# Optimization experiments

Hardware: AMD Instinct MI355X
Metric: run time of the kernel (lower is better)

The kernel has to match this reference:

```python
import jax, jax.numpy as jnp
import numpy as np

IN_F = 256
OUT_F = 256
HOP = 3
ALPHA = 0.2   # LeakyReLU negative slope
BETA = 0.5    # hop mixing coefficient
N = 50000
E = 1600000


def setup_inputs() -> dict:
    key = jax.random.key(0)
    k1, k2, k3, k4 = jax.random.split(key, 4)
    inp = jax.random.normal(k1, (N, IN_F), dtype=jnp.float32)
    k_edge_list = jax.random.randint(k2, (HOP, 2, E), 0, N, dtype=jnp.int32)
    # xavier_normal-ish scales
    W = jax.random.normal(k3, (IN_F * HOP, OUT_F), dtype=jnp.float32) * (1.414 * np.sqrt(2.0 / (IN_F * HOP + OUT_F)))
    a = jax.random.normal(k4, (1, 2 * OUT_F * HOP), dtype=jnp.float32) * (1.414 * np.sqrt(2.0 / (1 + 2 * OUT_F * HOP)))
    return {"input": inp, "k_edge_list": k_edge_list, "W": W, "a": a}


def reference(input, k_edge_list, W, a):
    n = input.shape[0]
    h_prime_return = jnp.zeros((n, OUT_F), dtype=input.dtype)
    for i in range(HOP - 1, -1, -1):
        # per-hop projection: h = input @ W[i*in : (i+1)*in]  -> [N, OUT_F]
        h = input @ W[i * IN_F:(i + 1) * IN_F, :]
        src = k_edge_list[i, 0]  # [E] row indices (scatter targets)
        dst = k_edge_list[i, 1]  # [E] col indices (gather sources)
        ai = a[0, 2 * i * OUT_F:(2 * i + 2) * OUT_F]
        # a_i . cat(h[src], h[dst]) == (h @ a_src)[src] + (h @ a_dst)[dst]
        s_src = h @ ai[:OUT_F]   # [N]
        s_dst = h @ ai[OUT_F:]   # [N]
        score = s_src[src] + s_dst[dst]                     # [E]
        edge_e = jnp.exp(-jax.nn.leaky_relu(score, ALPHA))  # [E]
        # sparse row-sum: spmm(A, ones)
        e_rowsum = jax.ops.segment_sum(edge_e, src, num_segments=n)          # [N]
        # weighted aggregate: spmm(A, h)
        h_prime = jax.ops.segment_sum(edge_e[:, None] * h[dst], src, num_segments=n)  # [N, OUT_F]
        h_prime = h_prime / e_rowsum[:, None]
        h_prime_return = (1.0 - BETA) * h_prime + BETA * h_prime_return
    return jax.nn.elu(h_prime_return)  # concat=True path
```

## Files before the change

kernel.cpp:

```cpp
#include <hip/hip_runtime.h>

#define N_NODES 50000
#define E_EDGES 1600000
#define HOPS    3
#define KDIM    256
#define NOUT    768
#define MPAD    50048
#define NPS     50176
#define NCB     196
#define NCB_ALL (NCB * HOPS)
#define HSTRIDE ((size_t)MPAD * 256)
#define PCAP    10240
#define RCAP    9216
#define SEB     4096

typedef unsigned short u16;
typedef __bf16 bf16x8 __attribute__((ext_vector_type(8)));
typedef float  f32x4  __attribute__((ext_vector_type(4)));

__device__ __forceinline__ u16 f2bf(float f) {
  unsigned u = __float_as_uint(f);
  u += 0x7fffu + ((u >> 16) & 1u);
  return (u16)(u >> 16);
}
__device__ __forceinline__ float bf2f(u16 h) {
  return __uint_as_float(((unsigned)h) << 16);
}

__device__ __forceinline__ void gl2lds16(const void* g, void* l) {
  __builtin_amdgcn_global_load_lds(
      (__attribute__((address_space(1))) void*)(g),
      (__attribute__((address_space(3))) void*)(l), 16, 0, 0);
}

__global__ __launch_bounds__(256) void conv_a(const float* __restrict__ in,
                                              u16* __restrict__ A) {
  int idx  = blockIdx.x * 256 + threadIdx.x;
  int base = idx * 4;
  int row  = base >> 8;
  ushort4 o;
  if (row < N_NODES) {
    float4 v = *(const float4*)(in + base);
    o.x = f2bf(v.x); o.y = f2bf(v.y); o.z = f2bf(v.z); o.w = f2bf(v.w);
  } else {
    o.x = 0; o.y = 0; o.z = 0; o.w = 0;
  }
  *(ushort4*)(A + base) = o;
}

__global__ __launch_bounds__(256) void conv_w(const float* __restrict__ W,
                                              u16* __restrict__ Bt) {
  __shared__ float tile[32][33];
  int h  = blockIdx.z;
  int c0 = blockIdx.x * 32;
  int k0 = blockIdx.y * 32;
  int x  = threadIdx.x & 31;
  int y0 = threadIdx.x >> 5;
#pragma unroll
  for (int i = 0; i < 4; ++i) {
    int k = k0 + y0 + i * 8;
    tile[y0 + i * 8][x] = W[(size_t)(h * 256 + k) * 256 + (c0 + x)];
  }
  __syncthreads();
#pragma unroll
  for (int i = 0; i < 4; ++i) {
    int c = c0 + y0 + i * 8;
    Bt[(size_t)(h * 256 + c) * 256 + (k0 + x)] = f2bf(tile[x][y0 + i * 8]);
  }
}

__global__ __launch_bounds__(256) void gemm_kernel(const u16* __restrict__ A,
                                                   const u16* __restrict__ B,
                                                   u16* __restrict__ H,
                                                   const float* __restrict__ a,
                                                   float* __restrict__ ssrc,
                                                   float* __restrict__ sdst) {
  __shared__ char lds[32768];
  int tid  = threadIdx.x;
  int lane = tid & 63;
  int w    = tid >> 6;
  int wm   = w >> 1, wn = w & 1;
  int r    = lane & 15, q = lane >> 4;
  int bm   = blockIdx.y * 128, bn = blockIdx.x * 128;

  const u16* Ag0 = A + (size_t)(bm + 2 * w * 16 + r) * KDIM + q * 8;
  const u16* Bg0 = B + (size_t)(bn + 2 * w * 16 + r) * KDIM + q * 8;

  f32x4 zero = {0.f, 0.f, 0.f, 0.f};
  f32x4 acc[4][4];
#pragma unroll
  for (int mt = 0; mt < 4; ++mt)
#pragma unroll
    for (int nt = 0; nt < 4; ++nt) acc[mt][nt] = zero;

#define STAGE(b, kt)                                                      \
  do {                                                                    \
    int ko = (kt) * 32;                                                   \
    char* As_ = lds + (b) * 16384;                                        \
    char* Bs_ = As_ + 8192;                                               \
    gl2lds16(Ag0 + ko,             As_ + (2 * w) * 1024);                 \
    gl2lds16(Ag0 + 16 * KDIM + ko, As_ + (2 * w + 1) * 1024);             \
    gl2lds16(Bg0 + ko,             Bs_ + (2 * w) * 1024);                 \
    gl2lds16(Bg0 + 16 * KDIM + ko, Bs_ + (2 * w + 1) * 1024);             \
  } while (0)

  STAGE(0, 0);
  __syncthreads();

  for (int kt = 0; kt < 8; ++kt) {
    int cur = kt & 1;
    if (kt < 7) STAGE(cur ^ 1, kt + 1);
    char* As = lds + cur * 16384;
    char* Bs = As + 8192;
    bf16x8 af[4], bfv[4];
#pragma unroll
    for (int mt = 0; mt < 4; ++mt)
      af[mt] = *(const bf16x8*)(As + (wm * 4 + mt) * 1024 + lane * 16);
#pragma unroll
    for (int nt = 0; nt < 4; ++nt)
      bfv[nt] = *(const bf16x8*)(Bs + (wn * 4 + nt) * 1024 + lane * 16);
#pragma unroll
    for (int mt = 0; mt < 4; ++mt)
#pragma unroll
      for (int nt = 0; nt < 4; ++nt)
        acc[mt][nt] = __builtin_amdgcn_mfma_f32_16x16x32_bf16(
            af[mt], bfv[nt], acc[mt][nt], 0, 0, 0);
    if (kt < 7) __syncthreads();
  }
#undef STAGE

  int hop = bn >> 8;
  int cbase = (bn & 255) + wn * 64 + r;
  float asv[4], adv[4];
#pragma unroll
  for (int nt = 0; nt < 4; ++nt) {
    asv[nt] = a[hop * 512 + cbase + nt * 16];
    adv[nt] = a[hop * 512 + 256 + cbase + nt * 16];
  }
#pragma unroll
  for (int mt = 0; mt < 4; ++mt)
#pragma unroll
    for (int rg = 0; rg < 4; ++rg) {
      float ps = 0.f, pd = 0.f;
#pragma unroll
      for (int nt = 0; nt < 4; ++nt) {
        float v = acc[mt][nt][rg];
        ps += v * asv[nt];
        pd += v * adv[nt];
      }
#pragma unroll
      for (int m = 1; m < 16; m <<= 1) {
        ps += __shfl_xor(ps, m);
        pd += __shfl_xor(pd, m);
      }
      if (r == 0) {
        int row = bm + wm * 64 + mt * 16 + q * 4 + rg;
        if (row < N_NODES) {
          atomicAdd(&ssrc[hop * NPS + row], ps);
          atomicAdd(&sdst[hop * NPS + row], pd);
        }
      }
    }

#pragma unroll
  for (int mt = 0; mt < 4; ++mt)
#pragma unroll
    for (int nt = 0; nt < 4; ++nt)
#pragma unroll
      for (int rg = 0; rg < 4; ++rg) {
        int row = bm + wm * 64 + mt * 16 + q * 4 + rg;
        int col = bn + wn * 64 + nt * 16 + r;
        int c = col & 255;
        H[hop * HSTRIDE + (size_t)row * 256 + c] = f2bf(acc[mt][nt][rg]);
      }
}

__global__ __launch_bounds__(256) void init_ccur(int* __restrict__ ccur) {
  int t = blockIdx.x * 256 + threadIdx.x;
  if (t < NCB_ALL) ccur[t] = t * PCAP;
}

__global__ __launch_bounds__(256) void split1_kernel(const int* __restrict__ kel,
                                                     const float* __restrict__ ssrc,
                                                     const float* __restrict__ sdst,
                                                     int* __restrict__ ccur,
                                                     int2* __restrict__ packed) {
  __shared__ int h[NCB];
  __shared__ int lcur[NCB];
  int t = threadIdx.x, hop = blockIdx.y;
  for (int i = t; i < NCB; i += 256) h[i] = 0;
  __syncthreads();
  const int* srcp = kel + (size_t)hop * 2 * E_EDGES;
  const int* dstp = srcp + E_EDGES;
  int e0 = blockIdx.x * SEB;
  int esrc[16], edst[16];
#pragma unroll
  for (int i = 0; i < 16; ++i) {
    int e = e0 + i * 256 + t;
    if (e < E_EDGES) {
      esrc[i] = srcp[e];
      edst[i] = dstp[e];
      atomicAdd(&h[esrc[i] >> 8], 1);
    } else {
      esrc[i] = -1;
    }
  }
  __syncthreads();
  for (int i = t; i < NCB; i += 256)
    if (h[i]) lcur[i] = atomicAdd(&ccur[hop * NCB + i], h[i]);
  __syncthreads();
#pragma unroll
  for (int i = 0; i < 16; ++i) {
    if (esrc[i] < 0) continue;
    int src = esrc[i], dst = edst[i];
    float s = ssrc[hop * NPS + src] + sdst[hop * NPS + dst];
    float lr = s > 0.0f ? s : 0.2f * s;
    float ee = __expf(-lr);
    int pos = atomicAdd(&lcur[src >> 8], 1);
    packed[pos] = make_int2(((src & 255) << 16) | dst, __float_as_int(ee));
  }
}

__global__ __launch_bounds__(1024) void fine_kernel(const int* __restrict__ ccur,
                                                    int2* __restrict__ packed,
                                                    int* __restrict__ offs,
                                                    int* __restrict__ counts) {
  __shared__ int h2[256];
  __shared__ int lc[256];
  __shared__ int wtot[4], wbase[4];
  int t = threadIdx.x;
  int b = blockIdx.x;
  int hop = b / NCB, bl = b % NCB;
  int base = b * PCAP;
  int cnt = ccur[b] - base;
  if (cnt > RCAP) cnt = RCAP;
  if (t < 256) h2[t] = 0;
  __syncthreads();
  int2 r0, r1, r2, r3, r4, r5, r6, r7, r8;
#define FLOAD(k, rv)                                                     \
  do {                                                                   \
    int idx = (k) * 1024 + t;                                            \
    if (idx < cnt) {                                                     \
      rv = packed[base + idx];                                           \
      atomicAdd(&h2[(rv.x >> 16) & 255], 1);                             \
    }                                                                    \
  } while (0)
  FLOAD(0, r0); FLOAD(1, r1); FLOAD(2, r2); FLOAD(3, r3); FLOAD(4, r4);
  FLOAD(5, r5); FLOAD(6, r6); FLOAD(7, r7); FLOAD(8, r8);
#undef FLOAD
  __syncthreads();
  int v = 0, s = 0;
  if (t < 256) {
    int lane = t & 63;
    v = h2[t];
    s = v;
#pragma unroll
    for (int d = 1; d < 64; d <<= 1) {
      int x = __shfl_up(s, d);
      if (lane >= d) s += x;
    }
    if (lane == 63) wtot[t >> 6] = s;
  }
  __syncthreads();
  if (t == 0) {
    int r = 0;
#pragma unroll
    for (int i = 0; i < 4; ++i) { wbase[i] = r; r += wtot[i]; }
  }
  __syncthreads();
  if (t < 256) {
    int ex = wbase[t >> 6] + s - v;
    int node = hop * NPS + bl * 256 + t;
    offs[node] = base + ex;
    counts[node] = v;
    lc[t] = ex;
  }
  __syncthreads();
#define FSCAT(k, rv)                                                     \
  do {                                                                   \
    int idx = (k) * 1024 + t;                                            \
    if (idx < cnt) {                                                     \
      int low = (rv.x >> 16) & 255;                                      \
      int rank = atomicAdd(&lc[low], 1);                                 \
      packed[base + rank] = make_int2(rv.x & 0xFFFF, rv.y);              \
    }                                                                    \
  } while (0)
  FSCAT(0, r0); FSCAT(1, r1); FSCAT(2, r2); FSCAT(3, r3); FSCAT(4, r4);
  FSCAT(5, r5); FSCAT(6, r6); FSCAT(7, r7); FSCAT(8, r8);
#undef FSCAT
}

__device__ __forceinline__ void accum8(float* a, float& rs, float ee, uint4 h) {
  rs += ee;
  a[0] += ee * __uint_as_float(h.x << 16);
  a[1] += ee * __uint_as_float(h.x & 0xffff0000u);
  a[2] += ee * __uint_as_float(h.y << 16);
  a[3] += ee * __uint_as_float(h.y & 0xffff0000u);
  a[4] += ee * __uint_as_float(h.z << 16);
  a[5] += ee * __uint_as_float(h.z & 0xffff0000u);
  a[6] += ee * __uint_as_float(h.w << 16);
  a[7] += ee * __uint_as_float(h.w & 0xffff0000u);
}

__global__ __launch_bounds__(256) void agg_all(const int* __restrict__ offs,
                                               const int* __restrict__ counts,
                                               const int2* __restrict__ packed,
                                               const u16* __restrict__ Hbf,
                                               float* __restrict__ out) {
  int lane = threadIdx.x & 63, wid = threadIdx.x >> 6;
  int half = lane >> 5, sub = lane & 31;
  int n = blockIdx.x * 4 + wid;
  if (n >= N_NODES) return;

  float r[8];
#pragma unroll
  for (int c = 0; c < 8; ++c) r[c] = 0.f;

#pragma unroll
  for (int hop = 0; hop < HOPS; ++hop) {
    const float wgt = hop == 0 ? 0.5f : (hop == 1 ? 0.25f : 0.125f);
    int start = offs[hop * NPS + n];
    int cnt = counts[hop * NPS + n];
    const int2* pk = packed + start;
    const u16* Hh = Hbf + hop * HSTRIDE + sub * 8;
    float a0[8], a1[8];
    float rs0 = 0.f, rs1 = 0.f;
#pragma unroll
    for (int c = 0; c < 8; ++c) { a0[c] = 0.f; a1[c] = 0.f; }

    int np = cnt >> 1;
    int j = 0;
    for (; j + 8 <= np; j += 8) {
      int2 p[8];
#pragma unroll
      for (int i = 0; i < 8; ++i) p[i] = pk[2 * (j + i) + half];
      uint4 h[8];
#pragma unroll
      for (int i = 0; i < 8; ++i) h[i] = *(const uint4*)(Hh + (size_t)p[i].x * 256);
#pragma unroll
      for (int i = 0; i < 8; ++i)
        accum8((i & 1) ? a1 : a0, (i & 1) ? rs1 : rs0, __int_as_float(p[i].y), h[i]);
    }
    for (; j < np; ++j) {
      int2 p = pk[2 * j + half];
      uint4 hv = *(const uint4*)(Hh + (size_t)p.x * 256);
      accum8(a0, rs0, __int_as_float(p.y), hv);
    }
    if (cnt & 1) {
      int2 p = pk[cnt - 1];
      float ee = half ? 0.f : __int_as_float(p.y);
      uint4 hv = *(const uint4*)(Hh + (size_t)p.x * 256);
      accum8(a1, rs1, ee, hv);
    }

    float rs = rs0 + rs1;
    rs += __shfl_xor(rs, 32);
    float inv = wgt / rs;
#pragma unroll
    for (int c = 0; c < 8; ++c) {
      float t = a0[c] + a1[c];
      t += __shfl_xor(t, 32);
      r[c] += t * inv;
    }
  }

  float* op = out + (size_t)n * 256 + sub * 8 + half * 4;
  float4 o;
  float v0 = r[half * 4 + 0], v1 = r[half * 4 + 1];
  float v2 = r[half * 4 + 2], v3 = r[half * 4 + 3];
  o.x = v0 > 0.f ? v0 : expm1f(v0);
  o.y = v1 > 0.f ? v1 : expm1f(v1);
  o.z = v2 > 0.f ? v2 : expm1f(v2);
  o.w = v3 > 0.f ? v3 : expm1f(v3);
  *(float4*)op = o;
}

extern "C" void kernel_launch(void* const* d_in, const int* in_sizes, int n_in,
                              void* d_out, int out_size, void* d_ws, size_t ws_size,
                              hipStream_t stream) {
  const float* input = (const float*)d_in[0];
  const int*   kel   = (const int*)d_in[1];
  const float* W     = (const float*)d_in[2];
  const float* a     = (const float*)d_in[3];
  float* out = (float*)d_out;

  char* ws = (char*)d_ws;
  size_t o = 0;
  u16* Abf = (u16*)(ws + o);   o += (size_t)MPAD * KDIM * 2;
  u16* Bt  = (u16*)(ws + o);   o += (size_t)NOUT * KDIM * 2;
  u16* Hbf = (u16*)(ws + o);   o += (size_t)MPAD * NOUT * 2;
  float* ssrc = (float*)(ws + o); o += (size_t)3 * NPS * 4;
  float* sdst = (float*)(ws + o); o += (size_t)3 * NPS * 4;
  int* counts = (int*)(ws + o);   o += (size_t)3 * NPS * 4;
  int* offs   = (int*)(ws + o);   o += (size_t)3 * NPS * 4;
  int* ccur   = (int*)(ws + o);   o += 4096;
  int2* packed = (int2*)(ws + o); o += (size_t)NCB_ALL * PCAP * 8 + 65536;

  hipMemsetAsync(ssrc, 0, (size_t)2 * 3 * NPS * 4, stream);

  conv_a<<<MPAD * KDIM / 1024, 256, 0, stream>>>(input, Abf);
  conv_w<<<dim3(8, 8, 3), 256, 0, stream>>>(W, Bt);
  init_ccur<<<3, 256, 0, stream>>>(ccur);
  gemm_kernel<<<dim3(NOUT / 128, MPAD / 128), 256, 0, stream>>>(Abf, Bt, Hbf,
                                                                a, ssrc, sdst);

  int nsplit = (E_EDGES + SEB - 1) / SEB;
  split1_kernel<<<dim3(nsplit, 3), 256, 0, stream>>>(kel, ssrc, sdst, ccur, packed);
  fine_kernel<<<NCB_ALL, 1024, 0, stream>>>(ccur, packed, offs, counts);

  agg_all<<<N_NODES / 4 + 1, 256, 0, stream>>>(offs, counts, packed, Hbf, out);
}
```

Before: 633.6 us.

## Defer edge score computation to fine bucketing kernel and shrink coarse intermediate

The coarse split kernel now writes only a 4-byte packed (local src, dst) word, into the bf16 input buffer that is free after the GEMM, instead of an 8-byte record holding the edge weight. The LeakyReLU/exp edge score is computed in the fine kernel, which caches the bucket's 256 source scores in LDS so only the destination score is gathered from global memory. This halves the coarse scatter traffic and replaces a random global source-score gather with an LDS read. The separate ccur init launch is folded into conv_a's first block, removing one kernel launch.

```diff
diff --git a/kernel.cpp b/kernel.cpp
--- a/kernel.cpp
+++ b/kernel.cpp
@@ -34,7 +34,11 @@
 }
 
 __global__ __launch_bounds__(256) void conv_a(const float* __restrict__ in,
-                                              u16* __restrict__ A) {
+                                              u16* __restrict__ A,
+                                              int* __restrict__ ccur) {
+  if (blockIdx.x == 0) {
+    for (int i = threadIdx.x; i < NCB_ALL; i += 256) ccur[i] = i * PCAP;
+  }
   int idx  = blockIdx.x * 256 + threadIdx.x;
   int base = idx * 4;
   int row  = base >> 8;
@@ -175,16 +179,9 @@
       }
 }
 
-__global__ __launch_bounds__(256) void init_ccur(int* __restrict__ ccur) {
-  int t = blockIdx.x * 256 + threadIdx.x;
-  if (t < NCB_ALL) ccur[t] = t * PCAP;
-}
-
 __global__ __launch_bounds__(256) void split1_kernel(const int* __restrict__ kel,
-                                                     const float* __restrict__ ssrc,
-                                                     const float* __restrict__ sdst,
                                                      int* __restrict__ ccur,
-                                                     int2* __restrict__ packed) {
+                                                     int* __restrict__ p1) {
   __shared__ int h[NCB];
   __shared__ int lcur[NCB];
   int t = threadIdx.x, hop = blockIdx.y;
@@ -212,19 +209,20 @@
 #pragma unroll
   for (int i = 0; i < 16; ++i) {
     if (esrc[i] < 0) continue;
-    int src = esrc[i], dst = edst[i];
-    float s = ssrc[hop * NPS + src] + sdst[hop * NPS + dst];
-    float lr = s > 0.0f ? s : 0.2f * s;
-    float ee = __expf(-lr);
+    int src = esrc[i];
     int pos = atomicAdd(&lcur[src >> 8], 1);
-    packed[pos] = make_int2(((src & 255) << 16) | dst, __float_as_int(ee));
+    p1[pos] = ((src & 255) << 16) | edst[i];
   }
 }
 
 __global__ __launch_bounds__(1024) void fine_kernel(const int* __restrict__ ccur,
+                                                    const int* __restrict__ p1,
+                                                    const float* __restrict__ ssrc,
+                                                    const float* __restrict__ sdst,
                                                     int2* __restrict__ packed,
                                                     int* __restrict__ offs,
                                                     int* __restrict__ counts) {
+  __shared__ float ss[256];
   __shared__ int h2[256];
   __shared__ int lc[256];
   __shared__ int wtot[4], wbase[4];
@@ -234,19 +232,29 @@
   int base = b * PCAP;
   int cnt = ccur[b] - base;
   if (cnt > RCAP) cnt = RCAP;
-  if (t < 256) h2[t] = 0;
-  __syncthreads();
-  int2 r0, r1, r2, r3, r4, r5, r6, r7, r8;
-#define FLOAD(k, rv)                                                     \
+  if (t < 256) {
+    h2[t] = 0;
+    ss[t] = ssrc[hop * NPS + bl * 256 + t];
+  }
+  __syncthreads();
+  const float* sd = sdst + hop * NPS;
+  int   r0, r1, r2, r3, r4, r5, r6, r7, r8;
+  float e0, e1, e2, e3, e4, e5, e6, e7, e8;
+#define FLOAD(k, rv, ev)                                                 \
   do {                                                                   \
     int idx = (k) * 1024 + t;                                            \
     if (idx < cnt) {                                                     \
-      rv = packed[base + idx];                                           \
-      atomicAdd(&h2[(rv.x >> 16) & 255], 1);                             \
+      rv = p1[base + idx];                                               \
+      int low = (rv >> 16) & 255;                                        \
+      atomicAdd(&h2[low], 1);                                            \
+      float s = ss[low] + sd[rv & 0xFFFF];                               \
+      float lr = s > 0.0f ? s : 0.2f * s;      \
+      ev = __expf(-lr);                                                  \
     }                                                                    \
   } while (0)
-  FLOAD(0, r0); FLOAD(1, r1); FLOAD(2, r2); FLOAD(3, r3); FLOAD(4, r4);
-  FLOAD(5, r5); FLOAD(6, r6); FLOAD(7, r7); FLOAD(8, r8);
+  FLOAD(0, r0, e0); FLOAD(1, r1, e1); FLOAD(2, r2, e2); FLOAD(3, r3, e3);
+  FLOAD(4, r4, e4); FLOAD(5, r5, e5); FLOAD(6, r6, e6); FLOAD(7, r7, e7);
+  FLOAD(8, r8, e8);
 #undef FLOAD
   __syncthreads();
   int v = 0, s = 0;
@@ -276,17 +284,18 @@
     lc[t] = ex;
   }
   __syncthreads();
-#define FSCAT(k, rv)                                                     \
+#define FSCAT(k, rv, ev)                                                 \
   do {                                                                   \
     int idx = (k) * 1024 + t;                                            \
     if (idx < cnt) {                                                     \
-      int low = (rv.x >> 16) & 255;                                      \
+      int low = (rv >> 16) & 255;                                        \
       int rank = atomicAdd(&lc[low], 1);                                 \
-      packed[base + rank] = make_int2(rv.x & 0xFFFF, rv.y);              \
+      packed[base + rank] = make_int2(rv & 0xFFFF, __float_as_int(ev));  \
     }                                                                    \
   } while (0)
-  FSCAT(0, r0); FSCAT(1, r1); FSCAT(2, r2); FSCAT(3, r3); FSCAT(4, r4);
-  FSCAT(5, r5); FSCAT(6, r6); FSCAT(7, r7); FSCAT(8, r8);
+  FSCAT(0, r0, e0); FSCAT(1, r1, e1); FSCAT(2, r2, e2); FSCAT(3, r3, e3);
+  FSCAT(4, r4, e4); FSCAT(5, r5, e5); FSCAT(6, r6, e6); FSCAT(7, r7, e7);
+  FSCAT(8, r8, e8);
 #undef FSCAT
 }
 
@@ -395,18 +404,19 @@
   int* offs   = (int*)(ws + o);   o += (size_t)3 * NPS * 4;
   int* ccur   = (int*)(ws + o);   o += 4096;
   int2* packed = (int2*)(ws + o); o += (size_t)NCB_ALL * PCAP * 8 + 65536;
+  int* p1 = (int*)Abf;
 
   hipMemsetAsync(ssrc, 0, (size_t)2 * 3 * NPS * 4, stream);
 
-  conv_a<<<MPAD * KDIM / 1024, 256, 0, stream>>>(input, Abf);
+  conv_a<<<MPAD * KDIM / 1024, 256, 0, stream>>>(input, Abf, ccur);
   conv_w<<<dim3(8, 8, 3), 256, 0, stream>>>(W, Bt);
-  init_ccur<<<3, 256, 0, stream>>>(ccur);
   gemm_kernel<<<dim3(NOUT / 128, MPAD / 128), 256, 0, stream>>>(Abf, Bt, Hbf,
                                                                 a, ssrc, sdst);
 
   int nsplit = (E_EDGES + SEB - 1) / SEB;
-  split1_kernel<<<dim3(nsplit, 3), 256, 0, stream>>>(kel, ssrc, sdst, ccur, packed);
-  fine_kernel<<<NCB_ALL, 1024, 0, stream>>>(ccur, packed, offs, counts);
+  split1_kernel<<<dim3(nsplit, 3), 256, 0, stream>>>(kel, ccur, p1);
+  fine_kernel<<<NCB_ALL, 1024, 0, stream>>>(ccur, p1, ssrc, sdst,
+                                            packed, offs, counts);
 
   agg_all<<<N_NODES / 4 + 1, 256, 0, stream>>>(offs, counts, packed, Hbf, out);
 }
```

New measurement: 623.1 us. About the same (-1.7%).
